# Performance work log

Hardware: AMD Instinct MI355X
Metric: run time of the kernel (lower is better)

## Reference

```python
import jax, jax.numpy as jnp
import numpy as np

N_NODES = 50000
N_EDGES = 600000
D_FEAT = 128


def setup_inputs() -> dict:
    key = jax.random.key(0)
    k1, k2, k3 = jax.random.split(key, 3)
    x = jax.random.normal(k1, (N_NODES, D_FEAT), dtype=jnp.float32)
    edge_index = jax.random.randint(k2, (2, N_EDGES), 0, N_NODES, dtype=jnp.int64)
    line_graph_val = jax.random.normal(k3, (N_EDGES,), dtype=jnp.float32)  # unused by module
    return {"x": x, "edge_index": edge_index, "line_graph_val": line_graph_val}


def reference(x, edge_index, line_graph_val):
    # edge_index is unpacked as (j, i): j = source, i = target (GCN convention)
    src = edge_index[0]  # j
    dst = edge_index[1]  # i
    n = x.shape[0]
    # deg = scatter-add of ones over target indices i
    deg = jax.ops.segment_sum(jnp.ones_like(src, dtype=x.dtype), dst, num_segments=n)
    # deg^{-1/2}; guard deg==0 (torch would give inf; isolated targets have no edges anyway)
    deg_inv_sqrt = jnp.where(deg > 0, deg ** -0.5, jnp.zeros_like(deg))
    norm = deg_inv_sqrt[src] * deg_inv_sqrt[dst]  # [E]
    # spmm(edge_index[[1,0]], norm, n, n, x): out[i] += norm_e * x[j]
    msg = norm[:, None] * x[src]  # [E, F]
    out = jax.ops.segment_sum(msg, dst, num_segments=n)  # [N, F]
    return jax.nn.relu(out)
```

## Files before the change

### kernel.cpp

```cpp
#include <hip/hip_runtime.h>


#define SORTB    256
#define CHUNKMAX 2368
#define NBP      512
#define BCAP     2048
#define GCAP     512

__device__ __forceinline__ int detect_is64(const unsigned int* w) {
    const int t = threadIdx.x & 63;
    unsigned long long m = __ballot(w[2 * t + 1] != 0u);
    return m == 0ull ? 1 : 0;
}

__device__ __forceinline__ int load_idx(const void* p, long long i, int is64) {
    return is64 ? (int)((const long long*)p)[i] : ((const int*)p)[i];
}

__device__ __forceinline__ unsigned short f2bf(float f) {
    unsigned u = __float_as_uint(f);
    unsigned r = (u + 0x7fffu + ((u >> 16) & 1u)) >> 16;
    return (unsigned short)r;
}

__global__ void k_zero_cur(int* cursor, int nb) {
    for (int i = threadIdx.x; i < nb; i += blockDim.x) cursor[i] = 0;
}

__global__ void __launch_bounds__(256) k_zero(int4* p, int n4) {
    const int stride = gridDim.x * blockDim.x;
    for (int i = blockIdx.x * blockDim.x + threadIdx.x; i < n4; i += stride)
        p[i] = make_int4(0, 0, 0, 0);
}


__global__ void __launch_bounds__(256) k_sort(const void* ei, int* cursor,
                                              unsigned int* __restrict__ buckets,
                                              int E, int CH) {
    __shared__ unsigned int raw[CHUNKMAX];
    __shared__ unsigned int srt[CHUNKMAX];
    __shared__ int hist[NBP];
    __shared__ int lbase[NBP];
    __shared__ int gbase[NBP];
    __shared__ int lcur[NBP];
    const int bid = blockIdx.x;
    const int t = threadIdx.x;
    for (int i = t; i < NBP; i += 256) hist[i] = 0;
    __syncthreads();
    const int is64 = detect_is64((const unsigned int*)ei);
    const int e0 = bid * CH;
    const int e1 = min(e0 + CH, E);
    const int nch = e1 - e0;
    for (int i = t; i < nch; i += 256) {
        const long long e = e0 + i;
        int s = load_idx(ei, e, is64);
        int d = load_idx(ei, (long long)E + e, is64);
        unsigned w = ((unsigned)d << 16) | (unsigned)s;
        raw[i] = w;
        atomicAdd(&hist[d >> 7], 1);
    }
    __syncthreads();
    if (t < 64) {
        const int base = t * 8;
        int v[8];
        int sum = 0;
        #pragma unroll
        for (int k = 0; k < 8; ++k) { v[k] = hist[base + k]; sum += v[k]; }
        int pre = sum;
        for (int off = 1; off < 64; off <<= 1) {
            int u = __shfl_up(pre, off);
            if (t >= off) pre += u;
        }
        pre -= sum;
        #pragma unroll
        for (int k = 0; k < 8; ++k) { lbase[base + k] = pre; pre += v[k]; }
    }
    __syncthreads();
    for (int b = t; b < NBP; b += 256) {
        const int c = hist[b];
        gbase[b] = c ? atomicAdd(&cursor[b], c) : 0;
        lcur[b] = lbase[b];
    }
    __syncthreads();
    for (int i = t; i < nch; i += 256) {
        const unsigned w = raw[i];
        const int p = atomicAdd(&lcur[w >> 23], 1);
        srt[p] = w;
    }
    __syncthreads();
    for (int i = t; i < nch; i += 256) {
        const unsigned w = srt[i];
        const int b = w >> 23;
        const int g = gbase[b] + (i - lbase[b]);
        if (g < BCAP) buckets[(size_t)b * BCAP + g] = w;
    }
}

__global__ void __launch_bounds__(256) k_conv(const unsigned int* __restrict__ buckets,
                                              const int* __restrict__ cursor,
                                              const float* __restrict__ x,
                                              unsigned short* __restrict__ xb, int n) {
    const int k = blockIdx.x;
    const int b = k >> 3;
    const int lo16 = (k & 7) * 16;
    __shared__ int h[16];
    __shared__ float sdinv[16];
    const int t = threadIdx.x;
    if (t < 16) h[t] = 0;
    __syncthreads();
    const int len = min(cursor[b], BCAP);
    const unsigned int* bb = buckets + (size_t)b * BCAP;
    for (int i = t; i < len; i += 256) {
        const int dl = ((bb[i] >> 16) & 127) - lo16;
        if ((unsigned)dl < 16u) atomicAdd(&h[dl], 1);
    }
    __syncthreads();
    if (t < 16) {
        const int c = h[t];
        sdinv[t] = (c > 0) ? rsqrtf((float)c) : 0.f;
    }
    __syncthreads();
    const long long base = (long long)k * 2048 + t * 8;
    if (base < (long long)n * 128) {
        const float w = sdinv[t >> 4];
        float4 a = *(const float4*)(x + base);
        float4 c = *(const float4*)(x + base + 4);
        union { unsigned short us[8]; uint4 v; } o;
        o.us[0] = f2bf(w * a.x); o.us[1] = f2bf(w * a.y);
        o.us[2] = f2bf(w * a.z); o.us[3] = f2bf(w * a.w);
        o.us[4] = f2bf(w * c.x); o.us[5] = f2bf(w * c.y);
        o.us[6] = f2bf(w * c.z); o.us[7] = f2bf(w * c.w);
        *(uint4*)(xb + base) = o.v;
    }
}

__global__ void __launch_bounds__(256) k_gather(const unsigned int* __restrict__ buckets,
                                                const int* __restrict__ cursor,
                                                const unsigned short* __restrict__ xb,
                                                float* __restrict__ out, int n) {
    const int b = blockIdx.x >> 3;
    const int oct = blockIdx.x & 7;
    __shared__ unsigned int kept[GCAP];
    __shared__ unsigned int srt[GCAP];
    __shared__ int h[16], st[17], lc[16];
    __shared__ int nk;
    const int t = threadIdx.x;
    if (t == 0) nk = 0;
    if (t < 16) h[t] = 0;
    __syncthreads();
    const int len = min(cursor[b], BCAP);
    const unsigned int* bb = buckets + (size_t)b * BCAP;
    for (int i = t; i < len; i += 256) {
        const unsigned w = bb[i];
        const int dl = (w >> 16) & 127;
        if ((dl >> 4) == oct) {
            const int p = atomicAdd(&nk, 1);
            if (p < GCAP) { kept[p] = w; atomicAdd(&h[dl & 15], 1); }
        }
    }
    __syncthreads();
    if (t < 16) {
        const int v = h[t];
        int pre = v;
        for (int off = 1; off < 16; off <<= 1) {
            int u = __shfl_up(pre, off);
            if (t >= off) pre += u;
        }
        pre -= v;
        st[t] = pre; lc[t] = pre;
        if (t == 15) st[16] = pre + v;
    }
    __syncthreads();
    const int nkk = min(nk, GCAP);
    for (int i = t; i < nkk; i += 256) {
        const unsigned w = kept[i];
        const int p = atomicAdd(&lc[(w >> 16) & 15], 1);
        srt[p] = w;
    }
    __syncthreads();
    const int g = t >> 4;
    const int lane = t & 15;
    const int node = b * 128 + oct * 16 + g;
    if (node >= n) return;
    int e = st[g];
    const int eend = st[g + 1];
    const int deg = eend - e;
    float acc[8] = {0.f, 0.f, 0.f, 0.f, 0.f, 0.f, 0.f, 0.f};

    auto addv = [&](uint4 v) {
        acc[0] += __uint_as_float(v.x << 16);
        acc[1] += __uint_as_float(v.x & 0xffff0000u);
        acc[2] += __uint_as_float(v.y << 16);
        acc[3] += __uint_as_float(v.y & 0xffff0000u);
        acc[4] += __uint_as_float(v.z << 16);
        acc[5] += __uint_as_float(v.z & 0xffff0000u);
        acc[6] += __uint_as_float(v.w << 16);
        acc[7] += __uint_as_float(v.w & 0xffff0000u);
    };

    for (; e + 7 < eend; e += 8) {
        int s[8];
        uint4 v[8];
        #pragma unroll
        for (int k = 0; k < 8; ++k) s[k] = srt[e + k] & 0xffff;
        #pragma unroll
        for (int k = 0; k < 8; ++k) v[k] = ((const uint4*)(xb + (size_t)s[k] * 128))[lane];
        #pragma unroll
        for (int k = 0; k < 8; ++k) addv(v[k]);
    }
    for (; e + 1 < eend; e += 2) {
        const int s0 = srt[e] & 0xffff, s1 = srt[e + 1] & 0xffff;
        uint4 v0 = ((const uint4*)(xb + (size_t)s0 * 128))[lane];
        uint4 v1 = ((const uint4*)(xb + (size_t)s1 * 128))[lane];
        addv(v0); addv(v1);
    }
    if (e < eend) {
        const int s0 = srt[e] & 0xffff;
        addv(((const uint4*)(xb + (size_t)s0 * 128))[lane]);
    }
    const float dd = (deg > 0) ? rsqrtf((float)deg) : 0.f;
    float4 o0, o1;
    o0.x = fmaxf(dd * acc[0], 0.f); o0.y = fmaxf(dd * acc[1], 0.f);
    o0.z = fmaxf(dd * acc[2], 0.f); o0.w = fmaxf(dd * acc[3], 0.f);
    o1.x = fmaxf(dd * acc[4], 0.f); o1.y = fmaxf(dd * acc[5], 0.f);
    o1.z = fmaxf(dd * acc[6], 0.f); o1.w = fmaxf(dd * acc[7], 0.f);
    float4* op = (float4*)(out + (size_t)node * 128);
    op[lane * 2] = o0;
    op[lane * 2 + 1] = o1;
}


__global__ void k_fill_direct(const void* ei, int* cnt, int* edges, int E, int cap) {
    const int is64 = detect_is64((const unsigned int*)ei);
    const int stride = gridDim.x * blockDim.x;
    for (int e = blockIdx.x * blockDim.x + threadIdx.x; e < E; e += stride) {
        int s = load_idx(ei, e, is64);
        int d = load_idx(ei, (long long)E + e, is64);
        int pos = atomicAdd(&cnt[d], 1);
        if (pos < cap) edges[(long long)d * cap + pos] = s;
    }
}

__global__ void __launch_bounds__(256) k_gather_pad(const float* __restrict__ x,
                                                    const int* __restrict__ edges,
                                                    const int* __restrict__ cnt,
                                                    float* __restrict__ out, int n, int cap) {
    const int node = blockIdx.x * 8 + (threadIdx.x >> 5);
    if (node >= n) return;
    const int lane = threadIdx.x & 31;
    const int m0 = cnt[node];
    const int m = min(m0, cap);
    const int* eb = edges + (long long)node * cap;
    float ax = 0.f, ay = 0.f, az = 0.f, aw = 0.f;
    int e = 0;
    for (; e + 3 < m; e += 4) {
        int s0 = eb[e], s1 = eb[e + 1], s2 = eb[e + 2], s3 = eb[e + 3];
        int c0 = cnt[s0], c1 = cnt[s1], c2 = cnt[s2], c3 = cnt[s3];
        float4 v0 = *(const float4*)(x + (long long)s0 * 128 + lane * 4);
        float4 v1 = *(const float4*)(x + (long long)s1 * 128 + lane * 4);
        float4 v2 = *(const float4*)(x + (long long)s2 * 128 + lane * 4);
        float4 v3 = *(const float4*)(x + (long long)s3 * 128 + lane * 4);
        float w0 = c0 > 0 ? rsqrtf((float)c0) : 0.f;
        float w1 = c1 > 0 ? rsqrtf((float)c1) : 0.f;
        float w2 = c2 > 0 ? rsqrtf((float)c2) : 0.f;
        float w3 = c3 > 0 ? rsqrtf((float)c3) : 0.f;
        ax += w0 * v0.x + w1 * v1.x + w2 * v2.x + w3 * v3.x;
        ay += w0 * v0.y + w1 * v1.y + w2 * v2.y + w3 * v3.y;
        az += w0 * v0.z + w1 * v1.z + w2 * v2.z + w3 * v3.z;
        aw += w0 * v0.w + w1 * v1.w + w2 * v2.w + w3 * v3.w;
    }
    for (; e < m; ++e) {
        int s0 = eb[e];
        int c0 = cnt[s0];
        float4 v0 = *(const float4*)(x + (long long)s0 * 128 + lane * 4);
        float w0 = c0 > 0 ? rsqrtf((float)c0) : 0.f;
        ax += w0 * v0.x; ay += w0 * v0.y; az += w0 * v0.z; aw += w0 * v0.w;
    }
    const float dd = m0 > 0 ? rsqrtf((float)m0) : 0.f;
    float4 rr;
    rr.x = fmaxf(dd * ax, 0.f); rr.y = fmaxf(dd * ay, 0.f);
    rr.z = fmaxf(dd * az, 0.f); rr.w = fmaxf(dd * aw, 0.f);
    *(float4*)(out + (long long)node * 128 + lane * 4) = rr;
}


__global__ void k_deg_simple(const void* ei, float* deg, int E) {
    const int is64 = detect_is64((const unsigned int*)ei);
    const int stride = gridDim.x * blockDim.x;
    for (int e = blockIdx.x * blockDim.x + threadIdx.x; e < E; e += stride)
        atomicAdd(&deg[load_idx(ei, (long long)E + e, is64)], 1.0f);
}
__global__ void k_dinv_simple(float* deg, int n) {
    int i = blockIdx.x * blockDim.x + threadIdx.x;
    if (i < n) { float d = deg[i]; deg[i] = d > 0.f ? rsqrtf(d) : 0.f; }
}
__global__ void k_scatter_atomic(const float* __restrict__ x, const void* ei,
                                 const float* __restrict__ dinv, float* out, int E) {
    const int is64 = detect_is64((const unsigned int*)ei);
    const int lane = threadIdx.x & 31;
    const int eslot = threadIdx.x >> 5;
    const int stride = gridDim.x * 8;
    for (int e = blockIdx.x * 8 + eslot; e < E; e += stride) {
        int s = load_idx(ei, e, is64);
        int d = load_idx(ei, (long long)E + e, is64);
        float norm = dinv[s] * dinv[d];
        float4 v = ((const float4*)(x + (long long)s * 128))[lane];
        float* o = out + (long long)d * 128 + lane * 4;
        atomicAdd(o + 0, norm * v.x); atomicAdd(o + 1, norm * v.y);
        atomicAdd(o + 2, norm * v.z); atomicAdd(o + 3, norm * v.w);
    }
}
__global__ void k_relu4(float4* out, int n4) {
    const int stride = gridDim.x * blockDim.x;
    for (int i = blockIdx.x * blockDim.x + threadIdx.x; i < n4; i += stride) {
        float4 v = out[i];
        v.x = fmaxf(v.x, 0.f); v.y = fmaxf(v.y, 0.f);
        v.z = fmaxf(v.z, 0.f); v.w = fmaxf(v.w, 0.f);
        out[i] = v;
    }
}

extern "C" void kernel_launch(void* const* d_in, const int* in_sizes, int n_in,
                              void* d_out, int out_size, void* d_ws, size_t ws_size,
                              hipStream_t stream) {
    const float* x = (const float*)d_in[0];
    const void* ei = d_in[1];
    const int D = 128;
    const int n = in_sizes[0] / D;
    const int E = in_sizes[1] / 2;

    char* ws = (char*)d_ws;
    size_t off = 0;
    auto alloc = [&](size_t bytes) {
        char* p = ws + off;
        off += (bytes + 255) & ~(size_t)255;
        return p;
    };
    auto al = [](size_t b) { return (b + 255) & ~(size_t)255; };

    const int nb = (n + 127) / 128;
    const int CH = (E + SORTB - 1) / SORTB;
    const size_t szCur = al((size_t)nb * 4);
    const size_t szBkt = al((size_t)nb * BCAP * 4);
    const size_t szXb  = al((size_t)n * D * 2);
    const size_t needS = szCur + szBkt + szXb;

    if (n <= 65536 && CH <= CHUNKMAX && nb <= NBP && ws_size >= needS) {
        int* cursor = (int*)alloc(szCur);
        unsigned int* buckets = (unsigned int*)alloc(szBkt);
        unsigned short* xb = (unsigned short*)alloc(szXb);

        k_zero_cur<<<1, 512, 0, stream>>>(cursor, nb);
        k_sort<<<SORTB, 256, 0, stream>>>(ei, cursor, buckets, E, CH);
        const int ntiles = (n * D + 2047) / 2048;
        k_conv<<<ntiles, 256, 0, stream>>>(buckets, cursor, x, xb, n);
        k_gather<<<nb * 8, 256, 0, stream>>>(buckets, cursor, xb, (float*)d_out, n);
        return;
    }

    auto needD = [&](int c) { return al((size_t)n * 4) + al((size_t)n * c * 4); };
    if (ws_size >= needD(48)) {
        int c = (ws_size >= needD(64)) ? 64 : 48;
        int* cnt   = (int*)alloc((size_t)n * 4);
        int* edges = (int*)alloc((size_t)n * c * 4);
        k_zero<<<(n / 4 + 255) / 256, 256, 0, stream>>>((int4*)cnt, n / 4);
        k_fill_direct<<<2048, 256, 0, stream>>>(ei, cnt, edges, E, c);
        k_gather_pad<<<(n + 7) / 8, 256, 0, stream>>>(x, edges, cnt, (float*)d_out, n, c);
        return;
    }

    float* deg = (float*)alloc((size_t)n * 4);
    hipMemsetAsync(deg, 0, (size_t)n * sizeof(float), stream);
    hipMemsetAsync(d_out, 0, (size_t)out_size * sizeof(float), stream);
    k_deg_simple<<<2048, 256, 0, stream>>>(ei, deg, E);
    k_dinv_simple<<<(n + 255) / 256, 256, 0, stream>>>(deg, n);
    k_scatter_atomic<<<4096, 256, 0, stream>>>(x, ei, deg, (float*)d_out, E);
    k_relu4<<<2048, 256, 0, stream>>>((float4*)d_out, out_size / 4);
}
```

Baseline: 61.22 us.

## Build CSR segments once per bucket and simplify gather kernel

Replaces the per-16-node conversion and gather kernels, which each rescanned a whole 2048-entry bucket, with one finalize kernel per 128-node bucket. That kernel counting-sorts the bucket by destination, writes 16-bit source arrays and per-node segment ranges, and converts x to scaled bf16. The gather kernel then reads its segment directly instead of filtering and sorting in shared memory. Redundant bucket scans drop, but the finalize launch has only about 391 blocks doing heavier work, and the sort kernel uses 512 blocks instead of 256.

```diff
diff --git a/kernel.cpp b/kernel.cpp
--- a/kernel.cpp
+++ b/kernel.cpp
@@ -1,11 +1,10 @@
 #include <hip/hip_runtime.h>
 
 
-#define SORTB    256
-#define CHUNKMAX 2368
+#define SORTB    512
+#define CHUNKMAX 1184
 #define NBP      512
 #define BCAP     2048
-#define GCAP     512
 
 __device__ __forceinline__ int detect_is64(const unsigned int* w) {
     const int t = threadIdx.x & 63;
@@ -96,94 +95,89 @@
     }
 }
 
-__global__ void __launch_bounds__(256) k_conv(const unsigned int* __restrict__ buckets,
-                                              const int* __restrict__ cursor,
-                                              const float* __restrict__ x,
-                                              unsigned short* __restrict__ xb, int n) {
-    const int k = blockIdx.x;
-    const int b = k >> 3;
-    const int lo16 = (k & 7) * 16;
-    __shared__ int h[16];
-    __shared__ float sdinv[16];
+__global__ void __launch_bounds__(256) k_finalize(const unsigned int* __restrict__ buckets,
+                                                  const int* __restrict__ cursor,
+                                                  const float* __restrict__ x,
+                                                  unsigned short* __restrict__ xb,
+                                                  unsigned short* __restrict__ srcs,
+                                                  int2* __restrict__ seg, int n) {
+    const int b = blockIdx.x;
+    __shared__ unsigned int raw[BCAP];
+    __shared__ unsigned short ss[BCAP];
+    __shared__ int hist[128], base[128], lcur[128];
+    __shared__ float sdinv[128];
     const int t = threadIdx.x;
-    if (t < 16) h[t] = 0;
-    __syncthreads();
-    const int len = min(cursor[b], BCAP);
-    const unsigned int* bb = buckets + (size_t)b * BCAP;
-    for (int i = t; i < len; i += 256) {
-        const int dl = ((bb[i] >> 16) & 127) - lo16;
-        if ((unsigned)dl < 16u) atomicAdd(&h[dl], 1);
-    }
-    __syncthreads();
-    if (t < 16) {
-        const int c = h[t];
-        sdinv[t] = (c > 0) ? rsqrtf((float)c) : 0.f;
-    }
-    __syncthreads();
-    const long long base = (long long)k * 2048 + t * 8;
-    if (base < (long long)n * 128) {
-        const float w = sdinv[t >> 4];
-        float4 a = *(const float4*)(x + base);
-        float4 c = *(const float4*)(x + base + 4);
-        union { unsigned short us[8]; uint4 v; } o;
-        o.us[0] = f2bf(w * a.x); o.us[1] = f2bf(w * a.y);
-        o.us[2] = f2bf(w * a.z); o.us[3] = f2bf(w * a.w);
-        o.us[4] = f2bf(w * c.x); o.us[5] = f2bf(w * c.y);
-        o.us[6] = f2bf(w * c.z); o.us[7] = f2bf(w * c.w);
-        *(uint4*)(xb + base) = o.v;
-    }
-}
-
-__global__ void __launch_bounds__(256) k_gather(const unsigned int* __restrict__ buckets,
-                                                const int* __restrict__ cursor,
-                                                const unsigned short* __restrict__ xb,
-                                                float* __restrict__ out, int n) {
-    const int b = blockIdx.x >> 3;
-    const int oct = blockIdx.x & 7;
-    __shared__ unsigned int kept[GCAP];
-    __shared__ unsigned int srt[GCAP];
-    __shared__ int h[16], st[17], lc[16];
-    __shared__ int nk;
-    const int t = threadIdx.x;
-    if (t == 0) nk = 0;
-    if (t < 16) h[t] = 0;
+    if (t < 128) hist[t] = 0;
     __syncthreads();
     const int len = min(cursor[b], BCAP);
     const unsigned int* bb = buckets + (size_t)b * BCAP;
     for (int i = t; i < len; i += 256) {
         const unsigned w = bb[i];
-        const int dl = (w >> 16) & 127;
-        if ((dl >> 4) == oct) {
-            const int p = atomicAdd(&nk, 1);
-            if (p < GCAP) { kept[p] = w; atomicAdd(&h[dl & 15], 1); }
-        }
-    }
-    __syncthreads();
-    if (t < 16) {
-        const int v = h[t];
-        int pre = v;
-        for (int off = 1; off < 16; off <<= 1) {
+        raw[i] = w;
+        atomicAdd(&hist[(w >> 16) & 127], 1);
+    }
+    __syncthreads();
+    if (t < 64) {
+        const int v0 = hist[2 * t], v1 = hist[2 * t + 1];
+        const int sum = v0 + v1;
+        int pre = sum;
+        for (int off = 1; off < 64; off <<= 1) {
             int u = __shfl_up(pre, off);
             if (t >= off) pre += u;
         }
-        pre -= v;
-        st[t] = pre; lc[t] = pre;
-        if (t == 15) st[16] = pre + v;
-    }
-    __syncthreads();
-    const int nkk = min(nk, GCAP);
-    for (int i = t; i < nkk; i += 256) {
-        const unsigned w = kept[i];
-        const int p = atomicAdd(&lc[(w >> 16) & 15], 1);
-        srt[p] = w;
-    }
-    __syncthreads();
-    const int g = t >> 4;
-    const int lane = t & 15;
-    const int node = b * 128 + oct * 16 + g;
+        pre -= sum;
+        base[2 * t] = pre;          base[2 * t + 1] = pre + v0;
+        lcur[2 * t] = pre;          lcur[2 * t + 1] = pre + v0;
+    }
+    __syncthreads();
+    if (t < 128) {
+        const int c = hist[t];
+        sdinv[t] = (c > 0) ? rsqrtf((float)c) : 0.f;
+        const int node = b * 128 + t;
+        if (node < n)
+            seg[node] = make_int2(b * BCAP + base[t], b * BCAP + base[t] + c);
+    }
+    __syncthreads();
+    for (int i = t; i < len; i += 256) {
+        const unsigned w = raw[i];
+        const int p = atomicAdd(&lcur[(w >> 16) & 127], 1);
+        ss[p] = (unsigned short)(w & 0xffffu);
+    }
+    __syncthreads();
+    unsigned short* so = srcs + (size_t)b * BCAP;
+    for (int i = t; i < len; i += 256) so[i] = ss[i];
+    const long long rowbase = (long long)b * 128;
+    #pragma unroll
+    for (int j = 0; j < 8; ++j) {
+        const int idx = j * 2048 + t * 8;
+        const int r = idx >> 7;
+        const int col = idx & 127;
+        const long long node = rowbase + r;
+        if (node < n) {
+            const float w = sdinv[r];
+            const float* xp = x + node * 128 + col;
+            float4 a = *(const float4*)xp;
+            float4 c4 = *(const float4*)(xp + 4);
+            union { unsigned short us[8]; uint4 v; } o;
+            o.us[0] = f2bf(w * a.x);  o.us[1] = f2bf(w * a.y);
+            o.us[2] = f2bf(w * a.z);  o.us[3] = f2bf(w * a.w);
+            o.us[4] = f2bf(w * c4.x); o.us[5] = f2bf(w * c4.y);
+            o.us[6] = f2bf(w * c4.z); o.us[7] = f2bf(w * c4.w);
+            *(uint4*)(xb + node * 128 + col) = o.v;
+        }
+    }
+}
+
+__global__ void __launch_bounds__(256) k_gather(const unsigned short* __restrict__ srcs,
+                                                const int2* __restrict__ seg,
+                                                const unsigned short* __restrict__ xb,
+                                                float* __restrict__ out, int n) {
+    const int node = blockIdx.x * 16 + (threadIdx.x >> 4);
     if (node >= n) return;
-    int e = st[g];
-    const int eend = st[g + 1];
+    const int lane = threadIdx.x & 15;
+    const int2 sg = seg[node];
+    int e = sg.x;
+    const int eend = sg.y;
     const int deg = eend - e;
     float acc[8] = {0.f, 0.f, 0.f, 0.f, 0.f, 0.f, 0.f, 0.f};
 
@@ -202,22 +196,20 @@
         int s[8];
         uint4 v[8];
         #pragma unroll
-        for (int k = 0; k < 8; ++k) s[k] = srt[e + k] & 0xffff;
+        for (int k = 0; k < 8; ++k) s[k] = srcs[e + k];
         #pragma unroll
         for (int k = 0; k < 8; ++k) v[k] = ((const uint4*)(xb + (size_t)s[k] * 128))[lane];
         #pragma unroll
         for (int k = 0; k < 8; ++k) addv(v[k]);
     }
     for (; e + 1 < eend; e += 2) {
-        const int s0 = srt[e] & 0xffff, s1 = srt[e + 1] & 0xffff;
+        const int s0 = srcs[e], s1 = srcs[e + 1];
         uint4 v0 = ((const uint4*)(xb + (size_t)s0 * 128))[lane];
         uint4 v1 = ((const uint4*)(xb + (size_t)s1 * 128))[lane];
         addv(v0); addv(v1);
     }
-    if (e < eend) {
-        const int s0 = srt[e] & 0xffff;
-        addv(((const uint4*)(xb + (size_t)s0 * 128))[lane]);
-    }
+    if (e < eend) addv(((const uint4*)(xb + (size_t)srcs[e] * 128))[lane]);
+
     const float dd = (deg > 0) ? rsqrtf((float)deg) : 0.f;
     float4 o0, o1;
     o0.x = fmaxf(dd * acc[0], 0.f); o0.y = fmaxf(dd * acc[1], 0.f);
@@ -342,19 +334,22 @@
     const int CH = (E + SORTB - 1) / SORTB;
     const size_t szCur = al((size_t)nb * 4);
     const size_t szBkt = al((size_t)nb * BCAP * 4);
+    const size_t szSrc = al((size_t)nb * BCAP * 2);
+    const size_t szSeg = al((size_t)n * 8);
     const size_t szXb  = al((size_t)n * D * 2);
-    const size_t needS = szCur + szBkt + szXb;
+    const size_t needS = szCur + szBkt + szSrc + szSeg + szXb;
 
     if (n <= 65536 && CH <= CHUNKMAX && nb <= NBP && ws_size >= needS) {
         int* cursor = (int*)alloc(szCur);
         unsigned int* buckets = (unsigned int*)alloc(szBkt);
+        unsigned short* srcs = (unsigned short*)alloc(szSrc);
+        int2* seg = (int2*)alloc(szSeg);
         unsigned short* xb = (unsigned short*)alloc(szXb);
 
         k_zero_cur<<<1, 512, 0, stream>>>(cursor, nb);
         k_sort<<<SORTB, 256, 0, stream>>>(ei, cursor, buckets, E, CH);
-        const int ntiles = (n * D + 2047) / 2048;
-        k_conv<<<ntiles, 256, 0, stream>>>(buckets, cursor, x, xb, n);
-        k_gather<<<nb * 8, 256, 0, stream>>>(buckets, cursor, xb, (float*)d_out, n);
+        k_finalize<<<nb, 256, 0, stream>>>(buckets, cursor, x, xb, srcs, seg, n);
+        k_gather<<<(n + 15) / 16, 256, 0, stream>>>(srcs, seg, xb, (float*)d_out, n);
         return;
     }
 
```

New measurement: 63.40 us. 1.04x slower.
